# Optimization experiments

Hardware: AMD Instinct MI355X
Metric: run time of the kernel (lower is better)

## Reference

```python
import jax, jax.numpy as jnp
import numpy as np

EMBED = 1024
HEADS = 16
HDIM = 64
FF = 4 * EMBED
EPS = 1e-5


def layer_norm(x, g, b):
    mu = jnp.mean(x, axis=-1, keepdims=True)
    var = jnp.var(x, axis=-1, keepdims=True)
    return (x - mu) * jax.lax.rsqrt(var + EPS) * g + b


def setup_inputs() -> dict:
    key = jax.random.key(0)
    ks = jax.random.split(key, 12)
    s = lambda fan_in: 1.0 / np.sqrt(fan_in)
    return {
        "x": jax.random.normal(ks[0], (2, 2048, EMBED), jnp.float32),
        "w_qkv": jax.random.uniform(ks[1], (EMBED, 3 * HEADS * HDIM), jnp.float32, -s(EMBED), s(EMBED)),
        "w_proj": jax.random.uniform(ks[2], (HEADS * HDIM, EMBED), jnp.float32, -s(HEADS * HDIM), s(HEADS * HDIM)),
        "b_proj": jax.random.uniform(ks[3], (EMBED,), jnp.float32, -s(HEADS * HDIM), s(HEADS * HDIM)),
        "w1": jax.random.uniform(ks[4], (EMBED, FF), jnp.float32, -s(EMBED), s(EMBED)),
        "b1": jax.random.uniform(ks[5], (FF,), jnp.float32, -s(EMBED), s(EMBED)),
        "w2": jax.random.uniform(ks[6], (FF, EMBED), jnp.float32, -s(FF), s(FF)),
        "b2": jax.random.uniform(ks[7], (EMBED,), jnp.float32, -s(FF), s(FF)),
        "g1": jnp.ones((EMBED,), jnp.float32),
        "be1": jnp.zeros((EMBED,), jnp.float32),
        "g2": jnp.ones((EMBED,), jnp.float32),
        "be2": jnp.zeros((EMBED,), jnp.float32),
    }


def reference(x, w_qkv, w_proj, b_proj, w1, b1, w2, b2, g1, be1, g2, be2):
    bs, seq, _ = x.shape
    # --- MHA on pre-norm ---
    h = layer_norm(x, g1, be1)
    qkv = h @ w_qkv  # [b, s, 3*H*D]
    qkv = qkv.reshape(bs, seq, HEADS, 3, HDIM)
    q = qkv[:, :, :, 0, :]  # [b, s, h, d]
    k = qkv[:, :, :, 1, :]
    v = qkv[:, :, :, 2, :]
    attn = jnp.einsum("bqhd,bkhd->bhqk", q, k) / np.sqrt(HDIM)
    causal = jnp.tril(jnp.ones((seq, seq), bool))
    attn = jnp.where(causal, attn, -jnp.inf)
    attn = jax.nn.softmax(attn, axis=-1)
    out = jnp.einsum("bhqk,bkhd->bhqd", attn, v)
    # Faithful to original bug: .view without transposing heads back.
    out = out.reshape(bs, seq, HEADS * HDIM)
    out = out @ w_proj + b_proj
    x = x + out
    # --- FFN on pre-norm ---
    h2 = layer_norm(x, g2, be2)
    ff = jax.nn.relu(h2 @ w1 + b1) @ w2 + b2
    return x + ff
```

## Files before the change

kernel.cpp:

```cpp
#include <hip/hip_runtime.h>
#include <cstdint>

#define EMBED 1024
#define HEADS 16
#define HDIM  64
#define SEQ   2048
#define BATCH 2
#define ROWS  (BATCH*SEQ)

typedef __bf16 bf16x8 __attribute__((ext_vector_type(8)));
typedef float  f32x4  __attribute__((ext_vector_type(4)));
typedef float  f32x16 __attribute__((ext_vector_type(16)));
typedef unsigned int uint32x2 __attribute__((ext_vector_type(2)));

__device__ __forceinline__ unsigned short f2bf(float f) {
    union { float f; uint32_t u; } v; v.f = f;
    uint32_t r = v.u + 0x7fffu + ((v.u >> 16) & 1u);
    return (unsigned short)(r >> 16);
}

__device__ __forceinline__ uint32_t cvtpk_bf16(float lo, float hi) {
    uint32_t r;
    asm("v_cvt_pk_bf16_f32 %0, %1, %2" : "=v"(r) : "v"(lo), "v"(hi));
    return r;
}

__device__ __forceinline__ float fexp2(float x) {
    float r;
    asm("v_exp_f32 %0, %1" : "=v"(r) : "v"(x));
    return r;
}

#define GLDS(src, dst) __builtin_amdgcn_global_load_lds( \
    (const __attribute__((address_space(1))) uint32_t*)(src), \
    (__attribute__((address_space(3))) uint32_t*)(dst), 16, 0, 0)

__global__ __launch_bounds__(256) void k_transpose_bf16(
    const float* __restrict__ in, unsigned short* __restrict__ out, int K, int N)
{
    __shared__ float tile[32][33];
    const int tx = threadIdx.x & 31, ty = threadIdx.x >> 5;
    const int n0 = blockIdx.x * 32, k0 = blockIdx.y * 32;
#pragma unroll
    for (int r = 0; r < 4; ++r)
        tile[ty + 8*r][tx] = in[(size_t)(k0 + ty + 8*r) * N + n0 + tx];
    __syncthreads();
#pragma unroll
    for (int r = 0; r < 4; ++r)
        out[(size_t)(n0 + ty + 8*r) * K + k0 + tx] = f2bf(tile[tx][ty + 8*r]);
}

__global__ __launch_bounds__(256) void k_layernorm(
    const float* __restrict__ x, const float* __restrict__ g, const float* __restrict__ b,
    unsigned short* __restrict__ h)
{
    const int row = blockIdx.x, t = threadIdx.x;
    float4 v = ((const float4*)(x + (size_t)row * EMBED))[t];
    float s = v.x + v.y + v.z + v.w;
    float q = v.x*v.x + v.y*v.y + v.z*v.z + v.w*v.w;
#pragma unroll
    for (int off = 32; off >= 1; off >>= 1) {
        s += __shfl_xor(s, off, 64);
        q += __shfl_xor(q, off, 64);
    }
    __shared__ float ss[4], sq[4];
    if ((t & 63) == 0) { ss[t >> 6] = s; sq[t >> 6] = q; }
    __syncthreads();
    s = ss[0] + ss[1] + ss[2] + ss[3];
    q = sq[0] + sq[1] + sq[2] + sq[3];
    const float mu  = s * (1.0f / EMBED);
    const float var = q * (1.0f / EMBED) - mu * mu;
    const float rs  = rsqrtf(var + 1e-5f);
    float4 gv = ((const float4*)g)[t];
    float4 bv = ((const float4*)b)[t];
    ushort4 o;
    o.x = f2bf((v.x - mu) * rs * gv.x + bv.x);
    o.y = f2bf((v.y - mu) * rs * gv.y + bv.y);
    o.z = f2bf((v.z - mu) * rs * gv.z + bv.z);
    o.w = f2bf((v.w - mu) * rs * gv.w + bv.w);
    ((ushort4*)(h + (size_t)row * EMBED))[t] = o;
}

template<int FLAGS, typename OutT>
__global__ __launch_bounds__(512) void k_gemm_bt(
    const unsigned short* __restrict__ A,
    const unsigned short* __restrict__ BT,
    const float* __restrict__ bias,
    const float* __restrict__ resid,
    OutT* __restrict__ C,
    int M, int N, int K)
{
    __shared__ uint4 ldsv[4096];
    char* base = (char*)ldsv;
    char* aL = base;
    char* bL = base + 16384;
    const int t = threadIdx.x, l = t & 63, w = t >> 6;
    const int pos = w & 3, kh = w >> 2;
    const int qr = pos >> 1, qc = pos & 1;
    const int g = l >> 4, c = l & 15;

    const int gx = gridDim.x;
    const int lin = blockIdx.y * gx + blockIdx.x;
    const int cpx = (gx * gridDim.y) >> 3;
    const int swz = (lin & 7) * cpx + (lin >> 3);
    const int row0 = (swz / gx) * 128, col0 = (swz % gx) * 128;

    const int swc = (((l & 7) ^ (l >> 3)) * 8);
    const int rA0 = w*16 + (l >> 3), rA1 = rA0 + 8;
    const unsigned short* aS0 = A  + (size_t)(row0 + rA0) * K + swc;
    const unsigned short* aS1 = A  + (size_t)(row0 + rA1) * K + swc;
    const unsigned short* bS0 = BT + (size_t)(col0 + rA0) * K + swc;
    const unsigned short* bS1 = BT + (size_t)(col0 + rA1) * K + swc;
    const int dst0 = w * 2048, dst1 = w * 2048 + 1024;

    f32x4 acc[4][4];
#pragma unroll
    for (int m = 0; m < 4; ++m)
#pragma unroll
        for (int n = 0; n < 4; ++n) acc[m][n] = f32x4{0.f, 0.f, 0.f, 0.f};

    auto stage = [&](int kt, int bo) {
        const size_t ko = (size_t)kt * 64;
        GLDS(aS0 + ko, aL + bo + dst0);
        GLDS(aS1 + ko, aL + bo + dst1);
        GLDS(bS0 + ko, bL + bo + dst0);
        GLDS(bS1 + ko, bL + bo + dst1);
    };
    auto compute = [&](int bo) {
        const int chb = ((kh*4 + g) ^ (c & 7)) * 16;
        bf16x8 af[4], bfr[4];
#pragma unroll
        for (int m = 0; m < 4; ++m)
            af[m] = *(const bf16x8*)(aL + bo + (qr*64 + m*16 + c) * 128 + chb);
#pragma unroll
        for (int n = 0; n < 4; ++n)
            bfr[n] = *(const bf16x8*)(bL + bo + (qc*64 + n*16 + c) * 128 + chb);
        __builtin_amdgcn_s_setprio(1);
#pragma unroll
        for (int m = 0; m < 4; ++m)
#pragma unroll
            for (int n = 0; n < 4; ++n)
                acc[m][n] = __builtin_amdgcn_mfma_f32_16x16x32_bf16(af[m], bfr[n], acc[m][n], 0, 0, 0);
        __builtin_amdgcn_s_setprio(0);
    };

    const int nkt = K >> 6;
    stage(0, 0);
    int bufo = 0;
    for (int kt = 0; kt < nkt - 1; ++kt) {
        stage(kt + 1, bufo ^ 32768);
        asm volatile("s_waitcnt vmcnt(4)" ::: "memory");
        __builtin_amdgcn_s_barrier();
        compute(bufo);
        asm volatile("s_waitcnt lgkmcnt(0)" ::: "memory");
        __builtin_amdgcn_s_barrier();
        bufo ^= 32768;
    }
    asm volatile("s_waitcnt vmcnt(0)" ::: "memory");
    __builtin_amdgcn_s_barrier();
    compute(bufo);

    asm volatile("s_waitcnt lgkmcnt(0)" ::: "memory");
    __builtin_amdgcn_s_barrier();
    if (kh) {
#pragma unroll
        for (int m = 0; m < 4; ++m)
#pragma unroll
            for (int n = 0; n < 4; ++n)
                *(f32x4*)(base + (((pos*16 + m*4 + n) * 64) + l) * 16) = acc[m][n];
    }
    asm volatile("s_waitcnt lgkmcnt(0)" ::: "memory");
    __builtin_amdgcn_s_barrier();

    if (!kh) {
#pragma unroll
        for (int m = 0; m < 4; ++m) {
            const int rb = row0 + qr*64 + m*16 + g*4;
#pragma unroll
            for (int n = 0; n < 4; ++n) {
                const f32x4 part = *(const f32x4*)(base + (((pos*16 + m*4 + n) * 64) + l) * 16);
                const int col = col0 + qc*64 + n*16 + c;
                float bv = 0.f;
                if constexpr ((FLAGS & 1) != 0) bv = bias[col];
#pragma unroll
                for (int j = 0; j < 4; ++j) {
                    float v = acc[m][n][j] + part[j] + bv;
                    if constexpr ((FLAGS & 2) != 0) v = fmaxf(v, 0.f);
                    if constexpr ((FLAGS & 4) != 0) v += resid[(size_t)(rb + j) * N + col];
                    if constexpr (sizeof(OutT) == 2) C[(size_t)(rb + j) * N + col] = (OutT)f2bf(v);
                    else                             C[(size_t)(rb + j) * N + col] = v;
                }
            }
        }
    }
}

template<int FLAGS, typename OutT>
__global__ __launch_bounds__(512) __attribute__((amdgpu_waves_per_eu(2, 2)))
void k_gemm256(
    const unsigned short* __restrict__ A,
    const unsigned short* __restrict__ BT,
    const float* __restrict__ bias,
    OutT* __restrict__ C,
    unsigned short* __restrict__ Qo,
    unsigned short* __restrict__ Ko,
    unsigned short* __restrict__ Vo,
    int M, int N, int K)
{
    __shared__ uint4 ldsv[8192];
    char* base = (char*)ldsv;
    const int t = threadIdx.x, l = t & 63, w = t >> 6;
    const int wr = w >> 2, wc = w & 3;
    const int g = l >> 4, c = l & 15;

    const int gx = gridDim.x;
    const int lin = blockIdx.y * gx + blockIdx.x;
    const int cpx = (gx * gridDim.y) >> 3;
    const int swz = (lin & 7) * cpx + (lin >> 3);
    const int row0 = (swz / gx) * 256, col0 = (swz % gx) * 256;

    const int sr = l >> 3, sc = l & 7;
    const int swk = (sc ^ sr) * 8;
    const unsigned short* aSr = A  + (size_t)(row0 + w*32 + sr) * K + swk;
    const unsigned short* bSr = BT + (size_t)(col0 + w*32 + sr) * K + swk;

    f32x4 acc[8][4];
#pragma unroll
    for (int m = 0; m < 8; ++m)
#pragma unroll
        for (int n = 0; n < 4; ++n) acc[m][n] = f32x4{0.f, 0.f, 0.f, 0.f};

    auto stage = [&](int kt, int bo) {
        const size_t ko = (size_t)kt * 64;
#pragma unroll
        for (int i = 0; i < 4; ++i) {
            GLDS(aSr + ko + (size_t)(i*8) * K, base + bo + (w*4 + i)*1024);
            GLDS(bSr + ko + (size_t)(i*8) * K, base + bo + 32768 + (w*4 + i)*1024);
        }
    };

    const int nkt = K >> 6;
    stage(0, 0);
    asm volatile("s_waitcnt vmcnt(0)" ::: "memory");
    __builtin_amdgcn_s_barrier();
    int bufo = 0;
    for (int kt = 0; kt < nkt; ++kt) {
        if (kt + 1 < nkt) stage(kt + 1, bufo ^ 65536);
        bf16x8 bfr[4][2];
#pragma unroll
        for (int n = 0; n < 4; ++n)
#pragma unroll
            for (int ks = 0; ks < 2; ++ks) {
                const int r = wc*64 + n*16 + c;
                bfr[n][ks] = *(const bf16x8*)(base + bufo + 32768 + r*128
                                              + (((ks*4 + g) ^ (c & 7)) * 16));
            }
#pragma unroll
        for (int p = 0; p < 4; ++p) {
            bf16x8 af[2][2];
#pragma unroll
            for (int mi = 0; mi < 2; ++mi)
#pragma unroll
                for (int ks = 0; ks < 2; ++ks) {
                    const int r = wr*128 + (p*2 + mi)*16 + c;
                    af[mi][ks] = *(const bf16x8*)(base + bufo + r*128
                                                  + (((ks*4 + g) ^ (c & 7)) * 16));
                }
            __builtin_amdgcn_s_setprio(1);
#pragma unroll
            for (int ks = 0; ks < 2; ++ks)
#pragma unroll
                for (int mi = 0; mi < 2; ++mi)
#pragma unroll
                    for (int n = 0; n < 4; ++n)
                        acc[p*2 + mi][n] = __builtin_amdgcn_mfma_f32_16x16x32_bf16(
                            af[mi][ks], bfr[n][ks], acc[p*2 + mi][n], 0, 0, 0);
            __builtin_amdgcn_s_setprio(0);
        }
        if (kt + 1 < nkt) {
            asm volatile("s_waitcnt vmcnt(0)" ::: "memory");
            __builtin_amdgcn_s_barrier();
            bufo ^= 65536;
        }
    }

    if constexpr ((FLAGS & 8) != 0) {
#pragma unroll
        for (int m = 0; m < 8; ++m) {
            const int rb = row0 + wr*128 + m*16 + g*4;
            const int b  = rb >> 11;
            const int q0 = rb & 2047;
#pragma unroll
            for (int n = 0; n < 4; ++n) {
                const int col = col0 + wc*64 + n*16 + c;
                const int hh  = col / 192;
                const int rem = col - hh * 192;
                const int tt  = rem >> 6;
                const int d   = rem & 63;
                const int bhh = b * HEADS + hh;
                if (tt == 2) {
                    const int st_e = q0 >> 6, kk = q0 & 63;
                    const int f_e  = (d >> 5) * 4 + (kk >> 4);
                    const int ln_e = ((kk >> 3) & 1) * 32 + (d & 31);
                    const int e0   = kk & 7;
                    ushort4 o;
                    o.x = f2bf(acc[m][n][0]); o.y = f2bf(acc[m][n][1]);
                    o.z = f2bf(acc[m][n][2]); o.w = f2bf(acc[m][n][3]);
                    *(ushort4*)(Vo + (size_t)bhh * (SEQ*HDIM) + st_e*4096 + f_e*512 + ln_e*8 + e0) = o;
                } else if (tt == 1) {
                    const int st_e = q0 >> 6;
                    const int f_e  = ((q0 >> 5) & 1) * 4 + (d >> 4);
                    const int lq_e = q0 & 31;
                    const int ln_b = ((d >> 3) & 1) * 32;
                    const int e_e  = d & 7;
                    unsigned short* dst = Ko + (size_t)bhh * (SEQ*HDIM) + st_e*4096 + f_e*512
                                             + (ln_b + lq_e)*8 + e_e;
#pragma unroll
                    for (int j = 0; j < 4; ++j)
                        dst[j*8] = f2bf(acc[m][n][j]);
                } else {
                    unsigned short* dst = Qo + ((size_t)bhh * SEQ + q0) * HDIM + d;
#pragma unroll
                    for (int j = 0; j < 4; ++j)
                        dst[(size_t)j * HDIM] = f2bf(acc[m][n][j]);
                }
            }
        }
    } else {
#pragma unroll
        for (int m = 0; m < 8; ++m) {
            const int rb = row0 + wr*128 + m*16 + g*4;
#pragma unroll
            for (int n = 0; n < 4; ++n) {
                const int col = col0 + wc*64 + n*16 + c;
                float bv = 0.f;
                if constexpr ((FLAGS & 1) != 0) bv = bias[col];
#pragma unroll
                for (int j = 0; j < 4; ++j) {
                    float v = acc[m][n][j] + bv;
                    if constexpr ((FLAGS & 2) != 0) v = fmaxf(v, 0.f);
                    if constexpr (sizeof(OutT) == 2) C[(size_t)(rb + j) * N + col] = (OutT)f2bf(v);
                    else                             C[(size_t)(rb + j) * N + col] = v;
                }
            }
        }
    }
}

__global__ __launch_bounds__(512) __attribute__((amdgpu_waves_per_eu(2, 2)))
void k_attention(
    const unsigned short* __restrict__ Qb,
    const unsigned short* __restrict__ Kf,
    const unsigned short* __restrict__ Vf,
    unsigned short* __restrict__ out)
{
    const int t = threadIdx.x, l = t & 63, w = t >> 6;
    const int lq = l & 31, hi = l >> 5;
    const int bid = blockIdx.x;
    const int sbid = (bid & 7) * 32 + (bid >> 3);
    const int bh = sbid >> 3, j = sbid & 7;
    const int qb = (w < 4) ? (4*j + w) : (63 - 4*j - (w - 4));
    const int q  = qb * 32 + lq;

    const unsigned short* Qh  = Qb + (size_t)bh * SEQ * HDIM;
    const unsigned short* Kfh = Kf + (size_t)bh * SEQ * HDIM + l*8;
    const unsigned short* Vfh = Vf + (size_t)bh * SEQ * HDIM + l*8;

    const bf16x8 qf0 = *(const bf16x8*)(Qh + (size_t)q * HDIM      + hi*8);
    const bf16x8 qf1 = *(const bf16x8*)(Qh + (size_t)q * HDIM + 16 + hi*8);
    const bf16x8 qf2 = *(const bf16x8*)(Qh + (size_t)q * HDIM + 32 + hi*8);
    const bf16x8 qf3 = *(const bf16x8*)(Qh + (size_t)q * HDIM + 48 + hi*8);

    f32x16 oT0, oT1;
#pragma unroll
    for (int i = 0; i < 16; ++i) { oT0[i] = 0.f; oT1[i] = 0.f; }
    float lacc0 = 0.f, lacc1 = 0.f, lacc2 = 0.f, lacc3 = 0.f;
    const float kSc = 0.18033688011112042f;
    const int nst = (qb >> 1) + 1;

    bf16x8 kA0, kA1, kA2, kA3, kA4, kA5, kA6, kA7;
    bf16x8 kB0, kB1, kB2, kB3, kB4, kB5, kB6, kB7;

#define LOADK(stv, KF) do {                                                     \
    const unsigned short* kp_ = Kfh + (size_t)(stv) * 4096;                     \
    KF##0 = *(const bf16x8*)(kp_ +    0); KF##1 = *(const bf16x8*)(kp_ +  512); \
    KF##2 = *(const bf16x8*)(kp_ + 1024); KF##3 = *(const bf16x8*)(kp_ + 1536); \
    KF##4 = *(const bf16x8*)(kp_ + 2048); KF##5 = *(const bf16x8*)(kp_ + 2560); \
    KF##6 = *(const bf16x8*)(kp_ + 3072); KF##7 = *(const bf16x8*)(kp_ + 3584); \
} while (0)

#define STEP(stv, KF) do {                                                      \
    const int kv0_ = (stv) * 64;                                                \
    const unsigned short* vp_ = Vfh + (size_t)(stv) * 4096;                     \
    bf16x8 vf0_ = *(const bf16x8*)(vp_ +    0), vf1_ = *(const bf16x8*)(vp_ +  512); \
    bf16x8 vf2_ = *(const bf16x8*)(vp_ + 1024), vf3_ = *(const bf16x8*)(vp_ + 1536); \
    bf16x8 vf4_ = *(const bf16x8*)(vp_ + 2048), vf5_ = *(const bf16x8*)(vp_ + 2560); \
    bf16x8 vf6_ = *(const bf16x8*)(vp_ + 3072), vf7_ = *(const bf16x8*)(vp_ + 3584); \
    f32x16 sA_, sB_;                                                            \
    _Pragma("unroll")                                                           \
    for (int i = 0; i < 16; ++i) { sA_[i] = 0.f; sB_[i] = 0.f; }               \
    __builtin_amdgcn_s_setprio(1);                                              \
    sA_ = __builtin_amdgcn_mfma_f32_32x32x16_bf16(KF##0, qf0, sA_, 0, 0, 0);    \
    sA_ = __builtin_amdgcn_mfma_f32_32x32x16_bf16(KF##1, qf1, sA_, 0, 0, 0);    \
    sA_ = __builtin_amdgcn_mfma_f32_32x32x16_bf16(KF##2, qf2, sA_, 0, 0, 0);    \
    sA_ = __builtin_amdgcn_mfma_f32_32x32x16_bf16(KF##3, qf3, sA_, 0, 0, 0);    \
    sB_ = __builtin_amdgcn_mfma_f32_32x32x16_bf16(KF##4, qf0, sB_, 0, 0, 0);    \
    sB_ = __builtin_amdgcn_mfma_f32_32x32x16_bf16(KF##5, qf1, sB_, 0, 0, 0);    \
    sB_ = __builtin_amdgcn_mfma_f32_32x32x16_bf16(KF##6, qf2, sB_, 0, 0, 0);    \
    sB_ = __builtin_amdgcn_mfma_f32_32x32x16_bf16(KF##7, qf3, sB_, 0, 0, 0);    \
    __builtin_amdgcn_s_setprio(0);                                              \
    float p_[32];                                                               \
    if ((stv) == nst - 1) {                                                     \
        _Pragma("unroll")                                                       \
        for (int r = 0; r < 16; ++r) {                                          \
            const int key_ = kv0_ + (r & 3) + 8*(r >> 2) + 4*hi;                \
            p_[r]      = (key_      <= q) ? fexp2(sA_[r] * kSc) : 0.f;          \
            p_[16 + r] = (key_ + 32 <= q) ? fexp2(sB_[r] * kSc) : 0.f;          \
        }                                                                       \
    } else {                                                                    \
        _Pragma("unroll")                                                       \
        for (int r = 0; r < 16; ++r) {                                          \
            p_[r]      = fexp2(sA_[r] * kSc);                                   \
            p_[16 + r] = fexp2(sB_[r] * kSc);                                   \
        }                                                                       \
    }                                                                           \
    _Pragma("unroll")                                                           \
    for (int i = 0; i < 32; i += 4) {                                           \
        lacc0 += p_[i]; lacc1 += p_[i+1]; lacc2 += p_[i+2]; lacc3 += p_[i+3];   \
    }                                                                           \
    bf16x8 pa_[4];                                                              \
    _Pragma("unroll")                                                           \
    for (int ks = 0; ks < 4; ++ks) {                                            \
        const int b8_ = ks * 8;                                                 \
        uint32x2 rA_ = __builtin_amdgcn_permlane32_swap(                        \
            cvtpk_bf16(p_[b8_+0], p_[b8_+1]), cvtpk_bf16(p_[b8_+4], p_[b8_+5]), false, false); \
        uint32x2 rB_ = __builtin_amdgcn_permlane32_swap(                        \
            cvtpk_bf16(p_[b8_+2], p_[b8_+3]), cvtpk_bf16(p_[b8_+6], p_[b8_+7]), false, false); \
        union { uint32_t u[4]; bf16x8 v; } pk_;                                 \
        pk_.u[0] = rA_[0]; pk_.u[1] = rB_[0]; pk_.u[2] = rA_[1]; pk_.u[3] = rB_[1]; \
        pa_[ks] = pk_.v;                                                        \
    }                                                                           \
    __builtin_amdgcn_s_setprio(1);                                              \
    oT0 = __builtin_amdgcn_mfma_f32_32x32x16_bf16(vf0_, pa_[0], oT0, 0, 0, 0);  \
    oT0 = __builtin_amdgcn_mfma_f32_32x32x16_bf16(vf1_, pa_[1], oT0, 0, 0, 0);  \
    oT0 = __builtin_amdgcn_mfma_f32_32x32x16_bf16(vf2_, pa_[2], oT0, 0, 0, 0);  \
    oT0 = __builtin_amdgcn_mfma_f32_32x32x16_bf16(vf3_, pa_[3], oT0, 0, 0, 0);  \
    oT1 = __builtin_amdgcn_mfma_f32_32x32x16_bf16(vf4_, pa_[0], oT1, 0, 0, 0);  \
    oT1 = __builtin_amdgcn_mfma_f32_32x32x16_bf16(vf5_, pa_[1], oT1, 0, 0, 0);  \
    oT1 = __builtin_amdgcn_mfma_f32_32x32x16_bf16(vf6_, pa_[2], oT1, 0, 0, 0);  \
    oT1 = __builtin_amdgcn_mfma_f32_32x32x16_bf16(vf7_, pa_[3], oT1, 0, 0, 0);  \
    __builtin_amdgcn_s_setprio(0);                                              \
} while (0)

    LOADK(0, kA);
    int st = 0;
    for (;;) {
        if (st + 1 < nst) LOADK(st + 1, kB);
        STEP(st, kA);
        if (++st >= nst) break;
        if (st + 1 < nst) LOADK(st + 1, kA);
        STEP(st, kB);
        if (++st >= nst) break;
    }
#undef LOADK
#undef STEP

    float lsum = (lacc0 + lacc1) + (lacc2 + lacc3);
    lsum += __shfl_xor(lsum, 32, 64);
    const float inv = 1.f / lsum;
    unsigned short* ob = out + ((size_t)bh * SEQ + q) * HDIM;
#pragma unroll
    for (int m2 = 0; m2 < 4; ++m2) {
        ushort4 o0, o1;
        o0.x = f2bf(oT0[m2*4+0] * inv); o0.y = f2bf(oT0[m2*4+1] * inv);
        o0.z = f2bf(oT0[m2*4+2] * inv); o0.w = f2bf(oT0[m2*4+3] * inv);
        o1.x = f2bf(oT1[m2*4+0] * inv); o1.y = f2bf(oT1[m2*4+1] * inv);
        o1.z = f2bf(oT1[m2*4+2] * inv); o1.w = f2bf(oT1[m2*4+3] * inv);
        *(ushort4*)(ob +      m2*8 + hi*4) = o0;
        *(ushort4*)(ob + 32 + m2*8 + hi*4) = o1;
    }
}

extern "C" void kernel_launch(void* const* d_in, const int* in_sizes, int n_in,
                              void* d_out, int out_size, void* d_ws, size_t ws_size,
                              hipStream_t stream)
{
    (void)in_sizes; (void)n_in; (void)out_size; (void)ws_size;
    const float* x      = (const float*)d_in[0];
    const float* w_qkv  = (const float*)d_in[1];
    const float* w_proj = (const float*)d_in[2];
    const float* b_proj = (const float*)d_in[3];
    const float* w1     = (const float*)d_in[4];
    const float* b1     = (const float*)d_in[5];
    const float* w2     = (const float*)d_in[6];
    const float* b2     = (const float*)d_in[7];
    const float* g1     = (const float*)d_in[8];
    const float* be1    = (const float*)d_in[9];
    const float* g2     = (const float*)d_in[10];
    const float* be2    = (const float*)d_in[11];

    char* ws = (char*)d_ws;
    size_t o = 0;
    auto take = [&](size_t bytes) -> char* {
        char* p = ws + o;
        o += (bytes + 255) & ~(size_t)255;
        return p;
    };
    unsigned short* wqkvT  = (unsigned short*)take(3072ull * 1024 * 2);
    unsigned short* wprojT = (unsigned short*)take(1024ull * 1024 * 2);
    unsigned short* w1T    = (unsigned short*)take(4096ull * 1024 * 2);
    unsigned short* w2T    = (unsigned short*)take(1024ull * 4096 * 2);
    unsigned short* h      = (unsigned short*)take(4096ull * 1024 * 2);
    unsigned short* Qb     = (unsigned short*)take(4096ull * 1024 * 2);
    unsigned short* Kfb    = (unsigned short*)take(4096ull * 1024 * 2);
    unsigned short* Vfb    = (unsigned short*)take(4096ull * 1024 * 2);
    unsigned short* attno  = (unsigned short*)take(4096ull * 1024 * 2);
    float*          x2     = (float*)take(4096ull * 1024 * 4);
    unsigned short* f1     = Qb;

    k_transpose_bf16<<<dim3(96, 32),  256, 0, stream>>>(w_qkv,  wqkvT,  1024, 3072);
    k_transpose_bf16<<<dim3(32, 32),  256, 0, stream>>>(w_proj, wprojT, 1024, 1024);
    k_transpose_bf16<<<dim3(128, 32), 256, 0, stream>>>(w1,     w1T,    1024, 4096);
    k_transpose_bf16<<<dim3(32, 128), 256, 0, stream>>>(w2,     w2T,    4096, 1024);

    k_layernorm<<<4096, 256, 0, stream>>>(x, g1, be1, h);
    k_gemm256<8, unsigned short><<<dim3(12, 16), 512, 0, stream>>>(
        h, wqkvT, nullptr, (unsigned short*)nullptr, Qb, Kfb, Vfb, ROWS, 3072, 1024);
    k_attention<<<256, 512, 0, stream>>>(Qb, Kfb, Vfb, attno);
    k_gemm_bt<5, float><<<dim3(8, 32), 512, 0, stream>>>(
        attno, wprojT, b_proj, x, x2, ROWS, 1024, 1024);
    k_layernorm<<<4096, 256, 0, stream>>>(x2, g2, be2, h);
    k_gemm256<3, unsigned short><<<dim3(16, 16), 512, 0, stream>>>(
        h, w1T, b1, f1, nullptr, nullptr, nullptr, ROWS, 4096, 1024);
    k_gemm_bt<5, float><<<dim3(8, 32), 512, 0, stream>>>(
        f1, w2T, b2, x2, (float*)d_out, ROWS, 1024, 4096);
}
```

Baseline: 187.8 us.

## Deepen GEMM LDS pipeline to four stages and merge weight transposes

Weight transposes for all four matrices are merged into a single launch to cut launch overhead. The projection/FFN-down GEMM switches from a double-buffered LDS scheme to a four-slot ring with prefetch distance two, removing the per-iteration trailing barrier. This is meant to hide global latency better, but it doubles LDS use to 128KB per block, which lowers occupancy.

```diff
diff --git a/kernel.cpp b/kernel.cpp
--- a/kernel.cpp
+++ b/kernel.cpp
@@ -35,12 +35,22 @@
     (const __attribute__((address_space(1))) uint32_t*)(src), \
     (__attribute__((address_space(3))) uint32_t*)(dst), 16, 0, 0)
 
-__global__ __launch_bounds__(256) void k_transpose_bf16(
-    const float* __restrict__ in, unsigned short* __restrict__ out, int K, int N)
+__global__ __launch_bounds__(256) void k_transpose_all(
+    const float* __restrict__ w_qkv, const float* __restrict__ w_proj,
+    const float* __restrict__ w1,    const float* __restrict__ w2,
+    unsigned short* __restrict__ wqkvT, unsigned short* __restrict__ wprojT,
+    unsigned short* __restrict__ w1T,   unsigned short* __restrict__ w2T)
 {
+    int b = blockIdx.x;
+    const float* in; unsigned short* out; int N, K, nx;
+    if (b < 3072)      {           in = w_qkv;  out = wqkvT;  K = 1024; N = 3072; nx = 96; }
+    else if (b < 4096) { b -= 3072; in = w_proj; out = wprojT; K = 1024; N = 1024; nx = 32; }
+    else if (b < 8192) { b -= 4096; in = w1;     out = w1T;    K = 1024; N = 4096; nx = 128; }
+    else               { b -= 8192; in = w2;     out = w2T;    K = 4096; N = 1024; nx = 32; }
+    const int n0 = (b % nx) * 32, k0 = (b / nx) * 32;
+
     __shared__ float tile[32][33];
     const int tx = threadIdx.x & 31, ty = threadIdx.x >> 5;
-    const int n0 = blockIdx.x * 32, k0 = blockIdx.y * 32;
 #pragma unroll
     for (int r = 0; r < 4; ++r)
         tile[ty + 8*r][tx] = in[(size_t)(k0 + ty + 8*r) * N + n0 + tx];
@@ -90,7 +100,7 @@
     OutT* __restrict__ C,
     int M, int N, int K)
 {
-    __shared__ uint4 ldsv[4096];
+    __shared__ uint4 ldsv[8192];
     char* base = (char*)ldsv;
     char* aL = base;
     char* bL = base + 16384;
@@ -146,19 +156,20 @@
 
     const int nkt = K >> 6;
     stage(0, 0);
-    int bufo = 0;
-    for (int kt = 0; kt < nkt - 1; ++kt) {
-        stage(kt + 1, bufo ^ 32768);
-        asm volatile("s_waitcnt vmcnt(4)" ::: "memory");
+    stage(1, 32768);
+    for (int kt = 0; kt < nkt; ++kt) {
+        const int bo = (kt & 3) * 32768;
+        if (kt + 2 < nkt) {
+            stage(kt + 2, ((kt + 2) & 3) * 32768);
+            asm volatile("s_waitcnt vmcnt(8)" ::: "memory");
+        } else if (kt + 1 < nkt) {
+            asm volatile("s_waitcnt vmcnt(4)" ::: "memory");
+        } else {
+            asm volatile("s_waitcnt vmcnt(0)" ::: "memory");
+        }
         __builtin_amdgcn_s_barrier();
-        compute(bufo);
-        asm volatile("s_waitcnt lgkmcnt(0)" ::: "memory");
-        __builtin_amdgcn_s_barrier();
-        bufo ^= 32768;
-    }
-    asm volatile("s_waitcnt vmcnt(0)" ::: "memory");
-    __builtin_amdgcn_s_barrier();
-    compute(bufo);
+        compute(bo);
+    }
 
     asm volatile("s_waitcnt lgkmcnt(0)" ::: "memory");
     __builtin_amdgcn_s_barrier();
@@ -518,10 +529,8 @@
     float*          x2     = (float*)take(4096ull * 1024 * 4);
     unsigned short* f1     = Qb;
 
-    k_transpose_bf16<<<dim3(96, 32),  256, 0, stream>>>(w_qkv,  wqkvT,  1024, 3072);
-    k_transpose_bf16<<<dim3(32, 32),  256, 0, stream>>>(w_proj, wprojT, 1024, 1024);
-    k_transpose_bf16<<<dim3(128, 32), 256, 0, stream>>>(w1,     w1T,    1024, 4096);
-    k_transpose_bf16<<<dim3(32, 128), 256, 0, stream>>>(w2,     w2T,    4096, 1024);
+    k_transpose_all<<<12288, 256, 0, stream>>>(
+        w_qkv, w_proj, w1, w2, wqkvT, wprojT, w1T, w2T);
 
     k_layernorm<<<4096, 256, 0, stream>>>(x, g1, be1, h);
     k_gemm256<8, unsigned short><<<dim3(12, 16), 512, 0, stream>>>(
```

Result: faster. 181.3 us (-3.5%).
